# Optimization experiments

Measured on AMD Instinct MI355X. Metric: run time of the kernel, lower is better.

The kernel has to match this reference:

```python
import jax, jax.numpy as jnp
import numpy as np

NH, NB, E, R, K, SU = 64, 384, 1024, 1024, 16, 64  # humans, boxes, enc size, repr size, cardinality, sub-repr
C, P, SPA = 256, 7, 36
NUM_ITER = 2


def _ln(x, g, b):
    m = jnp.mean(x, -1, keepdims=True)
    v = jnp.mean((x - m) ** 2, -1, keepdims=True)
    return (x - m) / jnp.sqrt(v + 1e-5) * g + b


def setup_inputs():
    key = jax.random.key(0)
    it = iter(jax.random.split(key, 48))
    def w(shape, scale=0.02):
        return jax.random.normal(next(it), shape, dtype=jnp.float32) * scale
    z = lambda *s: jnp.zeros(s, jnp.float32)
    return {
        "box_feats": jax.random.normal(next(it), (NB, C, P, P), dtype=jnp.float32),
        "spatial_raw": jax.random.uniform(next(it), (NH * NB, SPA), dtype=jnp.float32),
        "features3": jax.random.normal(next(it), (1, C, P, P), dtype=jnp.float32),
        "Wb1": w((C * P * P, E)), "bb1": z(E), "Wb2": w((E, E)), "bb2": z(E),
        "Ws1": w((SPA, 128)), "bs1": z(128), "Ws2": w((128, 256)), "bs2": z(256),
        "Ws3": w((256, 1024)), "bs3": z(1024),
        "Wadj": w((R, 1)), "badj": z(1),
        "gh": jnp.ones((E,), jnp.float32), "bh": z(E),
        "go": jnp.ones((E,), jnp.float32), "bo": z(E),
        "A1": w((K, 2 * E, SU)), "Ab1": z(K, SU), "A2": w((K, 1024, SU)), "Ab2": z(K, SU),
        "A3": w((K, SU, R)), "Ab3": z(K, R),
        "G1": w((K, 256, SU)), "Gb1": z(K, SU), "G2": w((K, 1024, SU)), "Gb2": z(K, SU),
        "G3": w((K, SU, R)), "Gb3": z(K, R),
        "S1": w((K, E, SU)), "Sb1": z(K, SU), "S2": w((K, 1024, SU)), "Sb2": z(K, SU),
        "S3": w((K, SU, R)), "Sb3": z(K, R),
        "O1": w((K, E, SU)), "Ob1": z(K, SU), "O2": w((K, 1024, SU)), "Ob2": z(K, SU),
        "O3": w((K, SU, R)), "Ob3": z(K, R),
        "n_h": NH,
    }


def _forward(box_feats, spatial_raw, features3, Wb1, bb1, Wb2, bb2, Ws1, bs1, Ws2, bs2, Ws3, bs3,
             Wadj, badj, gh, bh, go, bo, A1, Ab1, A2, Ab2, A3, Ab3, G1, Gb1, G2, Gb2, G3, Gb3,
             S1, Sb1, S2, Sb2, S3, Sb3, O1, Ob1, O2, Ob2, O3, Ob3, n_h):
    n = box_feats.shape[0]
    # box_head: Flatten -> Linear -> ReLU -> Linear -> ReLU
    enc = jax.nn.relu(jax.nn.relu(box_feats.reshape(n, -1) @ Wb1 + bb1) @ Wb2 + bb2)  # [n, E]
    h, o = enc[:n_h], enc
    # spatial_head MLP on flat pairs (pair p = i*n + j, human i, object j)
    sp = spatial_raw
    for W, b in ((Ws1, bs1), (Ws2, bs2), (Ws3, bs3)):
        sp = jax.nn.relu(sp @ W + b)                      # [n_h*n, 1024]
    spr = sp.reshape(n_h, n, -1)
    gfeat = features3.mean((2, 3))                        # AdaptiveAvgPool2d(1) -> [1, 256]

    def mbf(app, W1, b1, W2, b2, W3, b3):
        # MultiBranchFusion over flat pairs, K branches vectorized as batched GEMMs
        a = jnp.einsum('pa,kau->kpu', app, W1) + b1[:, None, :]
        s = jnp.einsum('ps,ksu->kpu', sp, W2) + b2[:, None, :]
        m = jax.nn.relu(a * s)                            # [K, P, sub]
        return jax.nn.relu(jnp.einsum('kpu,kur->pr', m, W3) + b3.sum(0))

    def pair_app(hh, oo):
        return jnp.concatenate([jnp.repeat(hh, n, axis=0), jnp.tile(oo, (n_h, 1))], axis=1)

    adj = jnp.ones((n_h, n), sp.dtype)
    for _ in range(NUM_ITER):
        wts = mbf(pair_app(h, o), A1, Ab1, A2, Ab2, A3, Ab3)      # [P, R]
        adj = (wts @ Wadj + badj).reshape(n_h, n)
        # MessageMBF object->subject (_forward_object_nodes): output [n_h, n, R], no final relu
        ao = jnp.einsum('na,kau->knu', o, O1) + Ob1[:, None, :]
        so = jnp.einsum('hns,ksu->khnu', spr, O2) + Ob2[:, None, None, :]
        m_o2s = jnp.einsum('khnu,kur->hnr', jax.nn.relu(ao[:, None] * so), O3) + Ob3.sum(0)
        h = _ln(h + jax.nn.relu(jnp.sum(jax.nn.softmax(adj, 1)[..., None] * m_o2s, axis=1)), gh, bh)
        # MessageMBF subject->object (_forward_human_nodes): output [n, n_h, R]
        ah = jnp.einsum('ha,kau->khu', h, S1) + Sb1[:, None, :]
        sh = jnp.einsum('hns,ksu->khnu', spr, S2) + Sb2[:, None, None, :]
        m_s2o = jnp.einsum('khnu,kur->nhr', jax.nn.relu(ah[:, :, None, :] * sh), S3) + Sb3.sum(0)
        o = _ln(o + jax.nn.relu(jnp.sum(jax.nn.softmax(adj.T, 1)[..., None] * m_s2o, axis=1)), go, bo)

    attn = mbf(pair_app(h, o), A1, Ab1, A2, Ab2, A3, Ab3)          # [P, R]
    gp = jnp.broadcast_to(gfeat, (sp.shape[0], gfeat.shape[1]))
    attn_g = mbf(gp, G1, Gb1, G2, Gb2, G3, Gb3)                    # [P, R]
    return jnp.concatenate([attn, attn_g], axis=1)                 # [P, 2R]


def reference(box_feats, spatial_raw, features3, Wb1, bb1, Wb2, bb2, Ws1, bs1, Ws2, bs2, Ws3, bs3,
              Wadj, badj, gh, bh, go, bo, A1, Ab1, A2, Ab2, A3, Ab3, G1, Gb1, G2, Gb2, G3, Gb3,
              S1, Sb1, S2, Sb2, S3, Sb3, O1, Ob1, O2, Ob2, O3, Ob3, n_h):
    return _forward(box_feats, spatial_raw, features3, Wb1, bb1, Wb2, bb2, Ws1, bs1, Ws2, bs2, Ws3, bs3,
                    Wadj, badj, gh, bh, go, bo, A1, Ab1, A2, Ab2, A3, Ab3, G1, Gb1, G2, Gb2, G3, Gb3,
                    S1, Sb1, S2, Sb2, S3, Sb3, O1, Ob1, O2, Ob2, O3, Ob3, n_h)
```

## Files before the change

### kernel.cpp

```cpp
#include <hip/hip_runtime.h>
#include <hip/hip_bf16.h>
#include <cstdint>
#include <cstddef>

#define NH    64
#define NB    384
#define EDIM  1024
#define PAIRS (NH*NB)
#define SPA   36

using in_t  = float;
using out_t = float;
using sb_t  = __hip_bfloat16;

typedef short bf16x8 __attribute__((ext_vector_type(8)));
typedef float f32x4  __attribute__((ext_vector_type(4)));

static __device__ __forceinline__ float cvt(float x){ return x; }
static __device__ __forceinline__ float cvt(__hip_bfloat16 x){ return __bfloat162float(x); }
static __device__ __forceinline__ void stv(float* p, float v){ *p = v; }
static __device__ __forceinline__ void stv(__hip_bfloat16* p, float v){ *p = __float2bfloat16(v); }

static __device__ __forceinline__ float b2f(unsigned short u){
  union { unsigned int i; float f; } x; x.i = ((unsigned int)u)<<16; return x.f;
}

typedef const __attribute__((address_space(1))) void* as1_t;
typedef __attribute__((address_space(3))) void* as3_t;
static __device__ __forceinline__ void gl_lds16(const void* g, void* l){
  __builtin_amdgcn_global_load_lds((as1_t)g, (as3_t)l, 16, 0, 0);
}

#define POOL_BB1   0
#define POOL_BB2   1024
#define POOL_BS1   2048
#define POOL_BS2   2176
#define POOL_BS3   2432
#define POOL_AB1   3456
#define POOL_GB1   4480
#define POOL_SB1   5504
#define POOL_OB1   6528
#define POOL_B2ALL 7552
#define POOL_AB3S  11648
#define POOL_GB3S  12672
#define POOL_SB3S  13696
#define POOL_OB3S  14720
#define POOL_GFEAT 15744
#define POOL_TOTAL 16000

template<int EPI, int RELU, typename TC>
__global__ __launch_bounds__(256)
void gemm_mfma(int M, int N, int KS, int lda, int ldb,
               const sb_t* __restrict__ A,
               const sb_t* __restrict__ Bt,
               const float* __restrict__ bias,
               TC* __restrict__ C, int ldc, int coff, long long strideCz,
               const float* __restrict__ Wadj,
               const float* __restrict__ ab3s,
               float* __restrict__ adjOut)
{
  __shared__ alignas(16) short lA[2][128*32];
  __shared__ alignas(16) short lB[2][128*32];
  const int tid = threadIdx.x;
  const int w = tid >> 6, l = tid & 63;
  const int m0 = blockIdx.x * 128, n0 = blockIdx.y * 128;
  const int wr = w >> 1, wc = w & 1;
  const int Koff = blockIdx.z * KS;

  const int srow = w*32 + (l>>2);
  const int scol = (l&3)*8;
  const sb_t* gA = A  + (size_t)(m0 + srow)*(size_t)lda + Koff + scol;
  const sb_t* gB = Bt + (size_t)(n0 + srow)*(size_t)ldb + Koff + scol;
  short* lA0 = &lA[0][(w*32)*32];
  short* lA1 = &lA[1][(w*32)*32];
  short* lB0 = &lB[0][(w*32)*32];
  short* lB1 = &lB[1][(w*32)*32];

  f32x4 acc[4][4];
  const f32x4 zz = {0.f,0.f,0.f,0.f};
  #pragma unroll
  for (int i=0;i<4;++i)
    #pragma unroll
    for (int j=0;j<4;++j) acc[i][j] = zz;

  const int fr  = l & 15;
  const int fko = (l >> 4) * 8;

  for (int k0 = 0; k0 < KS; k0 += 64) {
    gl_lds16(gA + k0,               lA0);
    gl_lds16(gA + k0 + 16*lda,      lA0 + 16*32);
    gl_lds16(gA + k0 + 32,          lA1);
    gl_lds16(gA + k0 + 32 + 16*lda, lA1 + 16*32);
    gl_lds16(gB + k0,               lB0);
    gl_lds16(gB + k0 + 16*ldb,      lB0 + 16*32);
    gl_lds16(gB + k0 + 32,          lB1);
    gl_lds16(gB + k0 + 32 + 16*ldb, lB1 + 16*32);
    __syncthreads();
    #pragma unroll
    for (int kh=0; kh<2; ++kh) {
      bf16x8 af[4], bfv[4];
      #pragma unroll
      for (int i=0;i<4;++i)
        af[i]  = *(const bf16x8*)&lA[kh][(wr*64 + i*16 + fr)*32 + fko];
      #pragma unroll
      for (int j=0;j<4;++j)
        bfv[j] = *(const bf16x8*)&lB[kh][(wc*64 + j*16 + fr)*32 + fko];
      #pragma unroll
      for (int i=0;i<4;++i)
        #pragma unroll
        for (int j=0;j<4;++j)
          acc[i][j] = __builtin_amdgcn_mfma_f32_16x16x32_bf16(af[i], bfv[j], acc[i][j], 0, 0, 0);
    }
    __syncthreads();
  }

  const int cn = l & 15;
  const int cr = (l >> 4) * 4;

  if (EPI == 1) {
    float part[4][4];
    #pragma unroll
    for (int i=0;i<4;++i)
      #pragma unroll
      for (int r=0;r<4;++r) part[i][r] = 0.f;
    #pragma unroll
    for (int j=0;j<4;++j) {
      const int col = n0 + wc*64 + j*16 + cn;
      const float wv = Wadj[col];
      const float bv = ab3s[col];
      #pragma unroll
      for (int i=0;i<4;++i)
        #pragma unroll
        for (int r=0;r<4;++r)
          part[i][r] += fmaxf(acc[i][j][r] + bv, 0.f) * wv;
    }
    #pragma unroll
    for (int m=1;m<16;m<<=1)
      #pragma unroll
      for (int i=0;i<4;++i)
        #pragma unroll
        for (int r=0;r<4;++r)
          part[i][r] += __shfl_xor(part[i][r], m, 64);
    if (cn == 0) {
      #pragma unroll
      for (int i=0;i<4;++i)
        #pragma unroll
        for (int r=0;r<4;++r)
          atomicAdd(&adjOut[m0 + wr*64 + i*16 + cr + r], part[i][r]);
    }
    return;
  }

  #pragma unroll
  for (int j=0;j<4;++j) {
    const int col = n0 + wc*64 + j*16 + cn;
    const float bv = (EPI==0 && bias) ? bias[col] : 0.f;
    #pragma unroll
    for (int i=0;i<4;++i) {
      #pragma unroll
      for (int r=0;r<4;++r) {
        const int row = m0 + wr*64 + i*16 + cr + r;
        float v = acc[i][j][r] + bv;
        if (RELU) v = fmaxf(v, 0.f);
        if (EPI == 2)
          stv(&C[(size_t)blockIdx.z*strideCz + (size_t)row*ldc + col], v);
        else
          stv(&C[(size_t)row*ldc + coff + col], v);
      }
    }
  }
}

template<int EPI, int RELU, typename TC>
__global__ __launch_bounds__(512, 2)
void gemm256(int M, int N, int K, int lda, int ldb,
             const sb_t* __restrict__ A,
             const sb_t* __restrict__ Bt,
             const float* __restrict__ bias,
             TC* __restrict__ C, int ldc, int coff,
             const float* __restrict__ Wadj,
             const float* __restrict__ ab3s,
             float* __restrict__ adjOut)
{
  __shared__ alignas(16) short sh[2][2][256*64];

  const int tid = threadIdx.x;
  const int w = tid >> 6, l = tid & 63;
  const int wr = w >> 2, wc = w & 3;

  const unsigned gx = gridDim.x, gy = gridDim.y;
  const unsigned nwg = gx * gy;
  const unsigned hwid = blockIdx.x + gx * blockIdx.y;
  const unsigned q = nwg >> 3, rr = nwg & 7;
  const unsigned xcd = hwid & 7, jj = hwid >> 3;
  const unsigned wg = (xcd < rr ? xcd*(q+1) : rr*(q+1) + (xcd-rr)*q) + jj;
  const int by = (int)(wg % gy), bx = (int)(wg / gy);
  const int m0 = bx * 256, n0 = by * 256;

  const int NT = K >> 6;

  const int lr = l >> 3;
  const int lch = ((l & 7) ^ lr) * 8;

  auto stage = [&](int p, int s, int t){
    short* lbA = &sh[p][0][0];
    short* lbB = &sh[p][1][0];
    const int k0 = t * 64;
    #pragma unroll
    for (int c=0;c<2;++c){
      const int g = (w<<1) + c;
      int row0; const sb_t* mat; int ld; int rb; short* dst;
      if (s==0){ row0 = g*8;                              mat=Bt; ld=ldb; rb=n0; dst=lbB; }
      else if (s==1){ row0 = 128 + g*8;                   mat=Bt; ld=ldb; rb=n0; dst=lbB; }
      else if (s==2){ row0 = (g<8)? g*8    : 128+(g-8)*8; mat=A;  ld=lda; rb=m0; dst=lbA; }
      else          { row0 = (g<8)? 64+g*8 : 192+(g-8)*8; mat=A;  ld=lda; rb=m0; dst=lbA; }
      gl_lds16(mat + (size_t)(rb + row0 + lr)*(size_t)ld + k0 + lch, dst + row0*64);
    }
  };

  const int fr = l & 15;
  const int fg = l >> 4;
  const int sx = fr & 7;
  const int x0 = ((0 + fg) ^ sx) * 8;
  const int x1 = ((4 + fg) ^ sx) * 8;
  const int oA = (wr*128 + fr) * 64;
  const int oB = (wc*64  + fr) * 64;

  f32x4 acc[8][4];
  const f32x4 zz = {0.f,0.f,0.f,0.f};
  #pragma unroll
  for (int i=0;i<8;++i)
    #pragma unroll
    for (int j=0;j<4;++j) acc[i][j] = zz;

#define G256_BAR()   __builtin_amdgcn_s_barrier()
#define G256_LGKM0() asm volatile("s_waitcnt lgkmcnt(0)" ::: "memory")
#define G256_LGKM8() asm volatile("s_waitcnt lgkmcnt(8)" ::: "memory")
#define G256_VM(n)   asm volatile("s_waitcnt vmcnt(" #n ")" ::: "memory")
#define G256_LOADA(ph)                                                   \
  af[0][0] = *(const bf16x8*)(sa + oA + (2*(ph)+0)*1024 + x0);           \
  af[0][1] = *(const bf16x8*)(sa + oA + (2*(ph)+0)*1024 + x1);           \
  af[1][0] = *(const bf16x8*)(sa + oA + (2*(ph)+1)*1024 + x0);           \
  af[1][1] = *(const bf16x8*)(sa + oA + (2*(ph)+1)*1024 + x1)
#define G256_MFMA(ph)                                                    \
  do { __builtin_amdgcn_s_setprio(1);                                    \
    _Pragma("unroll") for (int kk=0; kk<2; ++kk)                         \
    _Pragma("unroll") for (int ii=0; ii<2; ++ii)                         \
    _Pragma("unroll") for (int j=0; j<4; ++j)                            \
      acc[2*(ph)+ii][j] = __builtin_amdgcn_mfma_f32_16x16x32_bf16(       \
          af[ii][kk], bf[j][kk], acc[2*(ph)+ii][j], 0, 0, 0);            \
    __builtin_amdgcn_s_setprio(0); } while(0)

  stage(0,0,0); stage(0,1,0); stage(0,2,0); stage(0,3,0);
  G256_VM(4);
  if (NT > 1) {
    stage(1,0,1); stage(1,1,1); stage(1,2,1);
    G256_VM(6);
  } else {
    G256_VM(0);
  }
  G256_BAR();

  for (int t=0; t<NT; ++t) {
    const int cur = t & 1, pn = cur ^ 1;
    short* sa  = &sh[cur][0][0];
    short* sb2 = &sh[cur][1][0];
    bf16x8 bf[4][2], af[2][2];

    #pragma unroll
    for (int j=0;j<4;++j){
      bf[j][0] = *(const bf16x8*)(sb2 + oB + j*1024 + x0);
      bf[j][1] = *(const bf16x8*)(sb2 + oB + j*1024 + x1);
    }
    G256_LOADA(0);
    if (t+1 < NT) stage(pn, 3, t+1);
    G256_LGKM8();
    G256_BAR(); G256_LGKM0();
    G256_MFMA(0);
    G256_BAR();

    G256_LOADA(1);
    if (t+2 < NT) stage(cur, 0, t+2);
    G256_BAR(); G256_LGKM0();
    G256_MFMA(1);
    G256_BAR();

    G256_LOADA(2);
    if (t+2 < NT) stage(cur, 1, t+2);
    G256_BAR(); G256_LGKM0();
    G256_MFMA(2);
    G256_BAR();

    G256_LOADA(3);
    if (t+2 < NT) stage(cur, 2, t+2);
    G256_BAR(); G256_LGKM0();
    G256_MFMA(3);
    if (t+1 < NT) {
      if (t+2 < NT) { G256_VM(6); } else { G256_VM(0); }
      G256_BAR();
    }
  }

#undef G256_LOADA
#undef G256_MFMA

  const int cn = l & 15;
  const int cr = (l >> 4) * 4;

  if (EPI == 1) {
    float part[8][4];
    #pragma unroll
    for (int i=0;i<8;++i)
      #pragma unroll
      for (int r=0;r<4;++r) part[i][r] = 0.f;
    #pragma unroll
    for (int j=0;j<4;++j) {
      const int col = n0 + wc*64 + j*16 + cn;
      const float wv = Wadj[col];
      const float bv = ab3s[col];
      #pragma unroll
      for (int i=0;i<8;++i)
        #pragma unroll
        for (int r=0;r<4;++r)
          part[i][r] += fmaxf(acc[i][j][r] + bv, 0.f) * wv;
    }
    #pragma unroll
    for (int m=1;m<16;m<<=1)
      #pragma unroll
      for (int i=0;i<8;++i)
        #pragma unroll
        for (int r=0;r<4;++r)
          part[i][r] += __shfl_xor(part[i][r], m, 64);
    if (cn == 0) {
      #pragma unroll
      for (int i=0;i<8;++i)
        #pragma unroll
        for (int r=0;r<4;++r)
          atomicAdd(&adjOut[m0 + wr*128 + i*16 + cr + r], part[i][r]);
    }
    return;
  }

  if constexpr (sizeof(TC) == 2) {
    sb_t* ebs = (sb_t*)&sh[0][0][0];
    G256_LGKM0();
    G256_BAR();
    #pragma unroll
    for (int i=0;i<8;++i){
      const int lrow = wr*128 + i*16 + cr;
      #pragma unroll
      for (int j=0;j<4;++j){
        const int lcol = wc*64 + j*16 + cn;
        const float bv = bias ? bias[n0 + lcol] : 0.f;
        #pragma unroll
        for (int r=0;r<4;++r){
          float v = acc[i][j][r] + bv;
          if (RELU) v = fmaxf(v, 0.f);
          stv(&ebs[(lrow+r)*256 + lcol], v);
        }
      }
    }
    G256_LGKM0();
    G256_BAR();
    #pragma unroll
    for (int p=0;p<16;++p){
      const int lrow = p*16 + (tid>>5);
      const int sc = (tid&31)*8;
      bf16x8 v = *(const bf16x8*)((const short*)ebs + lrow*256 + sc);
      *(bf16x8*)((short*)C + (size_t)(m0+lrow)*ldc + coff + n0 + sc) = v;
    }
  } else {
    float* ebf = (float*)&sh[0][0][0];
    #pragma unroll
    for (int h=0; h<2; ++h){
      G256_LGKM0();
      G256_BAR();
      if (wr == h){
        #pragma unroll
        for (int i=0;i<8;++i){
          const int lrow = i*16 + cr;
          #pragma unroll
          for (int j=0;j<4;++j){
            const int lcol = wc*64 + j*16 + cn;
            const float bv = bias ? bias[n0 + lcol] : 0.f;
            #pragma unroll
            for (int r=0;r<4;++r){
              float v = acc[i][j][r] + bv;
              if (RELU) v = fmaxf(v, 0.f);
              ebf[(lrow+r)*256 + lcol] = v;
            }
          }
        }
      }
      G256_LGKM0();
      G256_BAR();
      #pragma unroll
      for (int p=0;p<16;++p){
        const int lrow = p*8 + (tid>>6);
        const int sc = (tid&63)*4;
        f32x4 v = *(const f32x4*)&ebf[lrow*256 + sc];
        *(f32x4*)((float*)C + (size_t)(m0 + h*128 + lrow)*ldc + coff + n0 + sc) = v;
      }
    }
  }
#undef G256_BAR
#undef G256_LGKM0
#undef G256_LGKM8
#undef G256_VM
}

template<typename TC>
__global__ __launch_bounds__(256)
void gemm_valu(int M, int N, int K,
               const in_t* __restrict__ S, int ldsS,
               const in_t* __restrict__ B, int ldb, long long strideB,
               const float* __restrict__ bias,
               TC* __restrict__ C, int ldc, int reluOut)
{
  __shared__ float As[16][65];
  __shared__ float Bs[16][68];
  const int z  = blockIdx.z;
  const in_t* Bz = B + (long long)z * strideB;
  const int m0 = blockIdx.x * 64;
  const int n0 = blockIdx.y * 64;
  const int tid = threadIdx.x;
  const int tx = tid & 15;
  const int ty = tid >> 4;

  float acc[4][4];
  #pragma unroll
  for (int i=0;i<4;++i)
    #pragma unroll
    for (int j=0;j<4;++j) acc[i][j]=0.f;

  const int kTiles = (K + 15) >> 4;
  for (int kt=0; kt<kTiles; ++kt) {
    const int k0 = kt << 4;
    #pragma unroll
    for (int q=0;q<4;++q) {
      const int p = m0 + ty + 16*q;
      const int c = k0 + tx;
      As[tx][ty+16*q] = (p < M && c < K) ? S[(size_t)p*ldsS + c] : 0.f;
    }
    {
      const int n = tid & 63;
      #pragma unroll
      for (int q=0;q<4;++q) {
        const int kk = (tid >> 6) + 4*q;
        const int gk = k0 + kk;
        const int gn = n0 + n;
        Bs[kk][n] = (gk < K && gn < N) ? Bz[(size_t)gk*ldb + gn] : 0.f;
      }
    }
    __syncthreads();
    #pragma unroll
    for (int kk=0; kk<16; ++kk) {
      float a[4], b[4];
      #pragma unroll
      for (int i=0;i<4;++i) a[i] = As[kk][ty + 16*i];
      #pragma unroll
      for (int j=0;j<4;++j) b[j] = Bs[kk][tx + 16*j];
      #pragma unroll
      for (int i=0;i<4;++i)
        #pragma unroll
        for (int j=0;j<4;++j) acc[i][j] += a[i]*b[j];
    }
    __syncthreads();
  }
  #pragma unroll
  for (int i=0;i<4;++i) {
    const int r = m0 + ty + 16*i;
    if (r >= M) continue;
    #pragma unroll
    for (int j=0;j<4;++j) {
      const int nn = n0 + tx + 16*j;
      if (nn >= N) continue;
      const int ccol = z*N + nn;
      float v = acc[i][j];
      if (bias) v += bias[ccol];
      if (reluOut) v = fmaxf(v, 0.f);
      stv(&C[(size_t)r*ldc + ccol], v);
    }
  }
}

struct Prep17 { const in_t* p[17]; };

__global__ __launch_bounds__(256)
void prep_kernel(Prep17 a, float* __restrict__ pool)
{
  const int len[17] = {1024,1024,128,256,1024,1024,1024,1024,1024,1024,1024,1024,1024,
                       1024,1024,1024,1024};
  const int off[17] = {POOL_BB1,POOL_BB2,POOL_BS1,POOL_BS2,POOL_BS3,POOL_AB1,
                       POOL_B2ALL+0,
                       POOL_GB1,
                       POOL_B2ALL+3072,
                       POOL_SB1,
                       POOL_B2ALL+2048,
                       POOL_OB1,
                       POOL_B2ALL+1024,
                       POOL_AB3S,POOL_GB3S,POOL_SB3S,POOL_OB3S};
  const int j = blockIdx.x;
  const in_t* src = a.p[j];
  const int L = len[j], o = off[j];
  for (int i = threadIdx.x; i < L; i += blockDim.x) {
    if (j < 13) {
      pool[o+i] = src[i];
    } else {
      float s = 0.f;
      for (int k=0;k<16;++k) s += src[k*1024 + i];
      pool[o+i] = s;
    }
  }
}

__global__ __launch_bounds__(64)
void gfeat_kernel(const in_t* __restrict__ f3, float* __restrict__ g)
{
  const int c = blockIdx.x;
  const int t = threadIdx.x;
  float s = (t < 49) ? f3[c*49 + t] : 0.f;
  #pragma unroll
  for (int o=32;o>0;o>>=1) s += __shfl_down(s, o, 64);
  if (t == 0) g[c] = s * (1.0f/49.0f);
}

__global__ __launch_bounds__(256)
void tcvt_kernel(const float* __restrict__ in, sb_t* __restrict__ outT, int R, int C)
{
  __shared__ float t[64][65];
  const int r0 = blockIdx.x*64, c0 = blockIdx.y*64;
  const int x = threadIdx.x & 63, y = threadIdx.x >> 6;
  #pragma unroll 4
  for (int q=0;q<16;++q){ const int rl = q*4 + y; t[rl][x] = in[(size_t)(r0+rl)*C + c0 + x]; }
  __syncthreads();
  #pragma unroll 4
  for (int q=0;q<16;++q){ const int cl = q*4 + y; stv(&outT[(size_t)(c0+cl)*R + r0 + x], t[x][cl]); }
}

__global__ __launch_bounds__(256)
void pack_kt_kernel(const float* __restrict__ W, sb_t* __restrict__ PT, int Cdim)
{
  __shared__ float t[64][65];
  const int c0 = blockIdx.x*64; const int k = blockIdx.y;
  const int x = threadIdx.x & 63, y = threadIdx.x >> 6;
  #pragma unroll 4
  for (int q=0;q<16;++q){ const int cl = q*4 + y; t[cl][x] = W[((size_t)k*Cdim + c0 + cl)*64 + x]; }
  __syncthreads();
  #pragma unroll 4
  for (int q=0;q<16;++q){ const int u = q*4 + y; stv(&PT[((size_t)k*64 + u)*Cdim + c0 + x], t[x][u]); }
}

__global__ void cvt_kernel(const float* __restrict__ in, sb_t* __restrict__ o, int n){
  const int i = blockIdx.x*256 + threadIdx.x;
  if (i < n) stv(&o[i], in[i]);
}

__global__ __launch_bounds__(256)
void combine4_kernel(const float* __restrict__ part, const float* __restrict__ bias,
                     sb_t* __restrict__ o)
{
  const int i = blockIdx.x*256 + threadIdx.x;
  const int c = i & 1023;
  float v = part[i] + part[i+393216] + part[i+2*393216] + part[i+3*393216] + bias[c];
  stv(&o[i], fmaxf(v, 0.f));
}

__global__ __launch_bounds__(256)
void combineN_kernel(const float* __restrict__ part, long long stride, int nz,
                     const float* __restrict__ bias, int N, int relu,
                     float* __restrict__ out)
{
  const int i = blockIdx.x*256 + threadIdx.x;
  float v = bias ? bias[i & (N-1)] : 0.f;
  for (int z=0; z<nz; ++z) v += part[(long long)z*stride + i];
  if (relu) v = fmaxf(v, 0.f);
  out[i] = v;
}

__global__ __launch_bounds__(256)
void encpost_kernel(const float* __restrict__ oB, sb_t* __restrict__ oBb,
                    float* __restrict__ hB, sb_t* __restrict__ hBb)
{
  const int p = blockIdx.x; const int c = blockIdx.y*256 + threadIdx.x;
  const float v = oB[(size_t)p*1024 + c];
  stv(&oBb[(size_t)p*1024+c], v);
  if (p < NH){ hB[(size_t)p*1024+c] = v; stv(&hBb[(size_t)p*1024+c], v); }
}

__global__ __launch_bounds__(256)
void mmake_kernel(const float* __restrict__ U, int hasU, int ldu,
                  const float* __restrict__ V, int hasV,
                  const sb_t* __restrict__ S, int ldS, int colOff,
                  sb_t* __restrict__ Mo)
{
  const int p = blockIdx.x;
  const int c = threadIdx.x * 4;
  const ushort4 sv = *(const ushort4*)((const unsigned short*)S + (size_t)p*ldS + colOff + c);
  float a0=0.f,a1=0.f,a2=0.f,a3=0.f;
  if (hasU){ const float* Up = U + (size_t)(p/NB)*ldu + c; a0=Up[0];a1=Up[1];a2=Up[2];a3=Up[3]; }
  if (hasV){ const float* Vp = V + (size_t)(p%NB)*1024 + c; a0+=Vp[0];a1+=Vp[1];a2+=Vp[2];a3+=Vp[3]; }
  __hip_bfloat16* mo = (__hip_bfloat16*)Mo + (size_t)p*1024 + c;
  mo[0] = __float2bfloat16(fmaxf(a0*b2f(sv.x),0.f));
  mo[1] = __float2bfloat16(fmaxf(a1*b2f(sv.y),0.f));
  mo[2] = __float2bfloat16(fmaxf(a2*b2f(sv.z),0.f));
  mo[3] = __float2bfloat16(fmaxf(a3*b2f(sv.w),0.f));
}

__global__ __launch_bounds__(512)
void smax_h_kernel(const float* __restrict__ adj, float* __restrict__ wh)
{
  __shared__ float red[512];
  const int hh = blockIdx.x, t = threadIdx.x;
  float av = (t < NB) ? adj[hh*NB + t] : -1e30f;
  red[t]=av; __syncthreads();
  for (int s=256;s>0;s>>=1){ if(t<s) red[t]=fmaxf(red[t],red[t+s]); __syncthreads(); }
  float mx = red[0]; __syncthreads();
  float e = (t < NB) ? __expf(av - mx) : 0.f;
  red[t]=e; __syncthreads();
  for (int s=256;s>0;s>>=1){ if(t<s) red[t]+=red[t+s]; __syncthreads(); }
  if (t < NB) wh[hh*NB + t] = e / red[0];
}

__global__ __launch_bounds__(64)
void smax_o_kernel(const float* __restrict__ adj, float* __restrict__ wo)
{
  const int n = blockIdx.x, t = threadIdx.x;
  float av = adj[t*NB + n];
  float mx = av;
  #pragma unroll
  for (int o=32;o>0;o>>=1) mx = fmaxf(mx, __shfl_xor(mx, o, 64));
  float e = __expf(av - mx);
  float s = e;
  #pragma unroll
  for (int o=32;o>0;o>>=1) s += __shfl_xor(s, o, 64);
  wo[n*64 + t] = e / s;
}

__global__ __launch_bounds__(128)
void wredH_kernel(const float* __restrict__ wh, const float* __restrict__ ao,
                  const sb_t* __restrict__ s4, int colOff, sb_t* __restrict__ mw)
{
  const int hh = blockIdx.x;
  const int c = blockIdx.y*128 + threadIdx.x;
  const unsigned short* sp = (const unsigned short*)s4 + (size_t)hh*NB*4096 + colOff + c;
  const float* whp = wh + hh*NB;
  float acc = 0.f;
  for (int n=0; n<NB; ++n)
    acc += whp[n] * fmaxf(ao[(size_t)n*1024 + c] * b2f(sp[(size_t)n*4096]), 0.f);
  stv(&mw[(size_t)hh*1024 + c], acc);
}

__global__ __launch_bounds__(128)
void wredO_kernel(const float* __restrict__ wo, const float* __restrict__ ah,
                  const sb_t* __restrict__ s4, int colOff, sb_t* __restrict__ mw)
{
  const int n = blockIdx.x;
  const int c = blockIdx.y*128 + threadIdx.x;
  const unsigned short* sp = (const unsigned short*)s4 + (size_t)n*4096 + colOff + c;
  const float* wop = wo + n*64;
  float acc = 0.f;
  for (int h=0; h<NH; ++h)
    acc += wop[h] * fmaxf(ah[(size_t)h*1024 + c] * b2f(sp[(size_t)h*NB*4096]), 0.f);
  stv(&mw[(size_t)n*1024 + c], acc);
}

static __device__ __forceinline__ float bsum(float v, float* red){
  const int t = threadIdx.x;
  red[t]=v; __syncthreads();
  for (int s=512;s>0;s>>=1){ if(t<s) red[t]+=red[t+s]; __syncthreads(); }
  float r = red[0]; __syncthreads();
  return r;
}

__global__ __launch_bounds__(1024)
void ln_update_kernel(const float* __restrict__ msg, const float* __restrict__ b3s,
                      const in_t* __restrict__ g, const in_t* __restrict__ b,
                      float* __restrict__ x, sb_t* __restrict__ xb)
{
  __shared__ float red[1024];
  const int row = blockIdx.x, t = threadIdx.x;
  float val = x[(size_t)row*1024 + t] + fmaxf(msg[(size_t)row*1024 + t] + b3s[t], 0.f);
  float mean = bsum(val, red) * (1.0f/1024.0f);
  float d = val - mean;
  float var = bsum(d*d, red) * (1.0f/1024.0f);
  float y = d * rsqrtf(var + 1e-5f) * g[t] + b[t];
  x[(size_t)row*1024 + t] = y;
  stv(&xb[(size_t)row*1024 + t], y);
}

template<int EPI, int RELU, typename TC>
static inline void launch_mfma(hipStream_t st, int M, int N, int KS, int lda, int ldb, int nz,
    const sb_t* A, const sb_t* Bt, const float* bias, TC* C, int ldc, int coff,
    long long strideCz, const float* Wadj, const float* ab3s, float* adjOut)
{
  dim3 g((unsigned)(M/128), (unsigned)(N/128), (unsigned)nz);
  hipLaunchKernelGGL((gemm_mfma<EPI,RELU,TC>), g, dim3(256), 0, st,
                     M,N,KS,lda,ldb,A,Bt,bias,C,ldc,coff,strideCz,Wadj,ab3s,adjOut);
}

template<int EPI, int RELU, typename TC>
static inline void launch_mfma256(hipStream_t st, int M, int N, int K, int lda, int ldb,
    const sb_t* A, const sb_t* Bt, const float* bias, TC* C, int ldc, int coff,
    const float* Wadj, const float* ab3s, float* adjOut)
{
  dim3 g((unsigned)(M/256), (unsigned)(N/256), 1);
  hipLaunchKernelGGL((gemm256<EPI,RELU,TC>), g, dim3(512), 0, st,
                     M,N,K,lda,ldb,A,Bt,bias,C,ldc,coff,Wadj,ab3s,adjOut);
}

static inline void launch_skinny(hipStream_t st, int M, int N, int K, int lda, int ldb, int nz,
    const sb_t* A, const sb_t* Bt, const float* bias, float* outp, int relu, float* scratch)
{
  launch_mfma<2,0,float>(st, M, N, K/nz, lda, ldb, nz, A, Bt, nullptr, scratch, N, 0,
                         (long long)M*N, nullptr, nullptr, nullptr);
  hipLaunchKernelGGL(combineN_kernel, dim3((unsigned)((M*N)/256)), dim3(256), 0, st,
                     scratch, (long long)M*N, nz, bias, N, relu, outp);
}

extern "C" void kernel_launch(void* const* d_in, const int* in_sizes, int n_in,
                              void* d_out, int out_size, void* d_ws, size_t ws_size,
                              hipStream_t stream)
{
  (void)in_sizes; (void)n_in; (void)out_size; (void)ws_size;

  const in_t* box  = (const in_t*)d_in[0];
  const in_t* spat = (const in_t*)d_in[1];
  const in_t* f3   = (const in_t*)d_in[2];
  const in_t* Wb1  = (const in_t*)d_in[3];
  const in_t* Wb2  = (const in_t*)d_in[5];
  const in_t* Ws1  = (const in_t*)d_in[7];
  const in_t* Ws2  = (const in_t*)d_in[9];
  const in_t* Ws3  = (const in_t*)d_in[11];
  const in_t* Wadj = (const in_t*)d_in[13];
  const in_t* gh   = (const in_t*)d_in[15];
  const in_t* bh   = (const in_t*)d_in[16];
  const in_t* go   = (const in_t*)d_in[17];
  const in_t* bo   = (const in_t*)d_in[18];
  const in_t* A1   = (const in_t*)d_in[19];
  const in_t* A2   = (const in_t*)d_in[21];
  const in_t* A3   = (const in_t*)d_in[23];
  const in_t* G1   = (const in_t*)d_in[25];
  const in_t* G2   = (const in_t*)d_in[27];
  const in_t* G3   = (const in_t*)d_in[29];
  const in_t* S1   = (const in_t*)d_in[31];
  const in_t* S2   = (const in_t*)d_in[33];
  const in_t* S3   = (const in_t*)d_in[35];
  const in_t* O1   = (const in_t*)d_in[37];
  const in_t* O2   = (const in_t*)d_in[39];
  const in_t* O3   = (const in_t*)d_in[41];
  out_t* out = (out_t*)d_out;

  char* wsb = (char*)d_ws;
  size_t off = 0;
  auto alloc = [&](size_t bytes)->void* {
    void* p = wsb + off; off += (bytes + 255) & ~(size_t)255; return p;
  };
  float* pool   = (float*)alloc((size_t)POOL_TOTAL*4);
  sb_t* Wb1T    = (sb_t*)alloc((size_t)1024*12544*2);
  sb_t* Wb2T    = (sb_t*)alloc((size_t)1024*1024*2);
  sb_t* Ws2T    = (sb_t*)alloc((size_t)256*128*2);
  sb_t* Ws3T    = (sb_t*)alloc((size_t)1024*256*2);
  sb_t* A3T     = (sb_t*)alloc((size_t)1024*1024*2);
  sb_t* O3T     = (sb_t*)alloc((size_t)1024*1024*2);
  sb_t* S3T     = (sb_t*)alloc((size_t)1024*1024*2);
  sb_t* G3T     = (sb_t*)alloc((size_t)1024*1024*2);
  sb_t* s2Tall  = (sb_t*)alloc((size_t)4096*1024*2);
  sb_t* O1T     = (sb_t*)alloc((size_t)1024*1024*2);
  sb_t* S1T     = (sb_t*)alloc((size_t)1024*1024*2);
  sb_t* A1T     = (sb_t*)alloc((size_t)1024*2048*2);
  sb_t* boxb    = (sb_t*)alloc((size_t)NB*12544*2);
  float* encP   = (float*)alloc((size_t)4*NB*EDIM*4);
  sb_t* encMidb = (sb_t*)alloc((size_t)NB*EDIM*2);
  float* oB     = (float*)alloc((size_t)NB*EDIM*4);
  sb_t* oBb     = (sb_t*)alloc((size_t)NB*EDIM*2);
  float* hB     = (float*)alloc((size_t)NH*EDIM*4);
  sb_t* hBb     = (sb_t*)alloc((size_t)128*EDIM*2);
  sb_t* sp1b    = (sb_t*)alloc((size_t)PAIRS*128*2);
  sb_t* sp2b    = (sb_t*)alloc((size_t)PAIRS*256*2);
  sb_t* spFb    = (sb_t*)alloc((size_t)PAIRS*EDIM*2);
  sb_t* mbuf    = spFb;
  sb_t* s4      = (sb_t*)alloc((size_t)PAIRS*4096*2);
  float* ahA    = (float*)alloc((size_t)128*EDIM*4);
  float* aoA    = (float*)alloc((size_t)NB*EDIM*4);
  float* aoO    = (float*)alloc((size_t)NB*EDIM*4);
  float* ahS    = (float*)alloc((size_t)128*EDIM*4);
  float* aGv    = (float*)alloc((size_t)EDIM*4);
  float* adj    = (float*)alloc((size_t)PAIRS*4);
  float* wh     = (float*)alloc((size_t)PAIRS*4);
  float* wo     = (float*)alloc((size_t)PAIRS*4);
  sb_t* mwH     = (sb_t*)alloc((size_t)128*EDIM*2);
  sb_t* mwO     = (sb_t*)alloc((size_t)NB*EDIM*2);
  float* hmsg   = (float*)alloc((size_t)128*EDIM*4);
  float* omsg   = (float*)alloc((size_t)NB*EDIM*4);

  Prep17 pp;
  const int prepIdx[17] = {4,6,8,10,12,20,22,26,28,32,34,38,40,24,30,36,42};
  for (int i=0;i<17;++i) pp.p[i] = (const in_t*)d_in[prepIdx[i]];
  hipLaunchKernelGGL(prep_kernel, dim3(17), dim3(256), 0, stream, pp, pool);
  hipLaunchKernelGGL(gfeat_kernel, dim3(256), dim3(64), 0, stream, f3, pool + POOL_GFEAT);

  hipLaunchKernelGGL(tcvt_kernel, dim3(196,16), dim3(256), 0, stream, Wb1, Wb1T, 12544, 1024);
  hipLaunchKernelGGL(tcvt_kernel, dim3(16,16),  dim3(256), 0, stream, Wb2, Wb2T, 1024, 1024);
  hipLaunchKernelGGL(tcvt_kernel, dim3(2,4),    dim3(256), 0, stream, Ws2, Ws2T, 128, 256);
  hipLaunchKernelGGL(tcvt_kernel, dim3(4,16),   dim3(256), 0, stream, Ws3, Ws3T, 256, 1024);
  hipLaunchKernelGGL(tcvt_kernel, dim3(16,16),  dim3(256), 0, stream, A3, A3T, 1024, 1024);
  hipLaunchKernelGGL(tcvt_kernel, dim3(16,16),  dim3(256), 0, stream, O3, O3T, 1024, 1024);
  hipLaunchKernelGGL(tcvt_kernel, dim3(16,16),  dim3(256), 0, stream, S3, S3T, 1024, 1024);
  hipLaunchKernelGGL(tcvt_kernel, dim3(16,16),  dim3(256), 0, stream, G3, G3T, 1024, 1024);

  hipLaunchKernelGGL(pack_kt_kernel, dim3(16,16), dim3(256), 0, stream, A2, s2Tall,            1024);
  hipLaunchKernelGGL(pack_kt_kernel, dim3(16,16), dim3(256), 0, stream, O2, s2Tall+1024*1024,  1024);
  hipLaunchKernelGGL(pack_kt_kernel, dim3(16,16), dim3(256), 0, stream, S2, s2Tall+2048*1024,  1024);
  hipLaunchKernelGGL(pack_kt_kernel, dim3(16,16), dim3(256), 0, stream, G2, s2Tall+3072*1024,  1024);
  hipLaunchKernelGGL(pack_kt_kernel, dim3(16,16), dim3(256), 0, stream, O1, O1T, 1024);
  hipLaunchKernelGGL(pack_kt_kernel, dim3(16,16), dim3(256), 0, stream, S1, S1T, 1024);
  hipLaunchKernelGGL(pack_kt_kernel, dim3(32,16), dim3(256), 0, stream, A1, A1T, 2048);

  hipLaunchKernelGGL(cvt_kernel, dim3((NB*12544)/256), dim3(256), 0, stream, box, boxb, NB*12544);

  launch_mfma<2,0,float>(stream, NB, EDIM, 3136, 12544, 12544, 4,
      boxb, Wb1T, nullptr, encP, EDIM, 0, (long long)NB*EDIM, nullptr, nullptr, nullptr);
  hipLaunchKernelGGL(combine4_kernel, dim3(NB*EDIM/256), dim3(256), 0, stream,
                     encP, pool+POOL_BB1, encMidb);
  launch_skinny(stream, NB, EDIM, EDIM, EDIM, EDIM, 4,
      encMidb, Wb2T, pool+POOL_BB2, oB, 1, encP);
  hipLaunchKernelGGL(encpost_kernel, dim3(NB,4), dim3(256), 0, stream, oB, oBb, hB, hBb);

  {
    dim3 g((PAIRS+63)/64, 2, 1);
    hipLaunchKernelGGL((gemm_valu<sb_t>), g, dim3(256), 0, stream,
        PAIRS, 128, SPA, spat, SPA, Ws1, 128, 0, pool+POOL_BS1, sp1b, 128, 1);
  }
  launch_mfma<0,1,sb_t>(stream, PAIRS, 256, 128, 128, 128, 1,
      sp1b, Ws2T, pool+POOL_BS2, sp2b, 256, 0, 0, nullptr, nullptr, nullptr);
  launch_mfma256<0,1,sb_t>(stream, PAIRS, EDIM, 256, 256, 256,
      sp2b, Ws3T, pool+POOL_BS3, spFb, EDIM, 0, nullptr, nullptr, nullptr);

  launch_mfma256<0,0,sb_t>(stream, PAIRS, 4096, EDIM, EDIM, EDIM,
      spFb, s2Tall, pool+POOL_B2ALL, s4, 4096, 0, nullptr, nullptr, nullptr);

  {
    dim3 g(1, 1, 16);
    hipLaunchKernelGGL((gemm_valu<float>), g, dim3(256), 0, stream,
        1, 64, 256, pool+POOL_GFEAT, 256, G1, 64, 16384, pool+POOL_GB1, aGv, EDIM, 0);
  }

  for (int it=0; it<2; ++it) {
    launch_skinny(stream, 128, EDIM, EDIM, EDIM, 2048, 8,
        hBb, A1T, pool+POOL_AB1, ahA, 0, encP);
    launch_skinny(stream, NB, EDIM, EDIM, EDIM, 2048, 4,
        oBb, A1T+1024, nullptr, aoA, 0, encP);
    hipLaunchKernelGGL(mmake_kernel, dim3(PAIRS), dim3(256), 0, stream,
                       ahA, 1, 1024, aoA, 1, s4, 4096, 0, mbuf);
    (void)hipMemsetAsync(adj, 0, (size_t)PAIRS*4, stream);
    launch_mfma256<1,0,float>(stream, PAIRS, EDIM, EDIM, EDIM, EDIM,
        mbuf, A3T, nullptr, (float*)nullptr, 0, 0, Wadj, pool+POOL_AB3S, adj);
    hipLaunchKernelGGL(smax_h_kernel, dim3(NH), dim3(512), 0, stream, adj, wh);
    hipLaunchKernelGGL(smax_o_kernel, dim3(NB), dim3(64), 0, stream, adj, wo);

    launch_skinny(stream, NB, EDIM, EDIM, EDIM, 1024, 4,
        oBb, O1T, pool+POOL_OB1, aoO, 0, encP);
    hipLaunchKernelGGL(wredH_kernel, dim3(NH,8), dim3(128), 0, stream,
                       wh, aoO, s4, 1024, mwH);
    launch_skinny(stream, 128, EDIM, EDIM, EDIM, 1024, 8,
        mwH, O3T, nullptr, hmsg, 0, encP);
    hipLaunchKernelGGL(ln_update_kernel, dim3(NH), dim3(1024), 0, stream,
                       hmsg, pool+POOL_OB3S, gh, bh, hB, hBb);

    launch_skinny(stream, 128, EDIM, EDIM, EDIM, 1024, 8,
        hBb, S1T, pool+POOL_SB1, ahS, 0, encP);
    hipLaunchKernelGGL(wredO_kernel, dim3(NB,8), dim3(128), 0, stream,
                       wo, ahS, s4, 2048, mwO);
    launch_skinny(stream, NB, EDIM, EDIM, EDIM, 1024, 4,
        mwO, S3T, nullptr, omsg, 0, encP);
    hipLaunchKernelGGL(ln_update_kernel, dim3(NB), dim3(1024), 0, stream,
                       omsg, pool+POOL_SB3S, go, bo, oB, oBb);
  }

  launch_skinny(stream, 128, EDIM, EDIM, EDIM, 2048, 8,
      hBb, A1T, pool+POOL_AB1, ahA, 0, encP);
  launch_skinny(stream, NB, EDIM, EDIM, EDIM, 2048, 4,
      oBb, A1T+1024, nullptr, aoA, 0, encP);
  hipLaunchKernelGGL(mmake_kernel, dim3(PAIRS), dim3(256), 0, stream,
                     ahA, 1, 1024, aoA, 1, s4, 4096, 0, mbuf);
  launch_mfma256<0,1,out_t>(stream, PAIRS, EDIM, EDIM, EDIM, EDIM,
      mbuf, A3T, pool+POOL_AB3S, out, 2048, 0, nullptr, nullptr, nullptr);

  hipLaunchKernelGGL(mmake_kernel, dim3(PAIRS), dim3(256), 0, stream,
                     aGv, 1, 0, nullptr, 0, s4, 4096, 3072, mbuf);
  launch_mfma256<0,1,out_t>(stream, PAIRS, EDIM, EDIM, EDIM, EDIM,
      mbuf, G3T, pool+POOL_GB3S, out, 2048, 1024, nullptr, nullptr, nullptr);
}
```

Baseline: 1.481 ms.

## Switch 256-tile GEMM to 32x32x16 MFMA, swizzle epilogue LDS, split-K 7

The 256x256 GEMM kernel now uses 32x32x16 bf16 MFMA instructions with 16-float accumulators instead of 16x16x32. It reorganizes the fragment loads, the adjacency epilogue reduction, and the output staging to match the new accumulator layout. Epilogue LDS writes and reads are XOR-swizzled to reduce bank conflicts. Separately, the box-head first GEMM is split seven ways instead of four, and a generic combine kernel replaces the specialized one. This trades more partial-sum traffic for more parallelism.

```diff
diff --git a/kernel.cpp b/kernel.cpp
--- a/kernel.cpp
+++ b/kernel.cpp
@@ -15,6 +15,7 @@
 
 typedef short bf16x8 __attribute__((ext_vector_type(8)));
 typedef float f32x4  __attribute__((ext_vector_type(4)));
+typedef float f32x16 __attribute__((ext_vector_type(16)));
 
 static __device__ __forceinline__ float cvt(float x){ return x; }
 static __device__ __forceinline__ float cvt(__hip_bfloat16 x){ return __bfloat162float(x); }
@@ -218,37 +219,35 @@
     }
   };
 
-  const int fr = l & 15;
-  const int fg = l >> 4;
+  const int fr = l & 31;
+  const int fg = l >> 5;
   const int sx = fr & 7;
-  const int x0 = ((0 + fg) ^ sx) * 8;
-  const int x1 = ((4 + fg) ^ sx) * 8;
+  const int kx[4] = { (((0)+fg) ^ sx) * 8, (((2)+fg) ^ sx) * 8,
+                      (((4)+fg) ^ sx) * 8, (((6)+fg) ^ sx) * 8 };
   const int oA = (wr*128 + fr) * 64;
   const int oB = (wc*64  + fr) * 64;
 
-  f32x4 acc[8][4];
-  const f32x4 zz = {0.f,0.f,0.f,0.f};
+  f32x16 acc[4][2];
   #pragma unroll
-  for (int i=0;i<8;++i)
-    #pragma unroll
-    for (int j=0;j<4;++j) acc[i][j] = zz;
+  for (int i=0;i<4;++i)
+    #pragma unroll
+    for (int j=0;j<2;++j)
+      #pragma unroll
+      for (int r=0;r<16;++r) acc[i][j][r] = 0.f;
 
 #define G256_BAR()   __builtin_amdgcn_s_barrier()
 #define G256_LGKM0() asm volatile("s_waitcnt lgkmcnt(0)" ::: "memory")
 #define G256_LGKM8() asm volatile("s_waitcnt lgkmcnt(8)" ::: "memory")
 #define G256_VM(n)   asm volatile("s_waitcnt vmcnt(" #n ")" ::: "memory")
 #define G256_LOADA(ph)                                                   \
-  af[0][0] = *(const bf16x8*)(sa + oA + (2*(ph)+0)*1024 + x0);           \
-  af[0][1] = *(const bf16x8*)(sa + oA + (2*(ph)+0)*1024 + x1);           \
-  af[1][0] = *(const bf16x8*)(sa + oA + (2*(ph)+1)*1024 + x0);           \
-  af[1][1] = *(const bf16x8*)(sa + oA + (2*(ph)+1)*1024 + x1)
+  _Pragma("unroll") for (int kk=0; kk<4; ++kk)                           \
+    af[kk] = *(const bf16x8*)(sa + oA + (ph)*2048 + kx[kk]);
 #define G256_MFMA(ph)                                                    \
   do { __builtin_amdgcn_s_setprio(1);                                    \
-    _Pragma("unroll") for (int kk=0; kk<2; ++kk)                         \
-    _Pragma("unroll") for (int ii=0; ii<2; ++ii)                         \
-    _Pragma("unroll") for (int j=0; j<4; ++j)                            \
-      acc[2*(ph)+ii][j] = __builtin_amdgcn_mfma_f32_16x16x32_bf16(       \
-          af[ii][kk], bf[j][kk], acc[2*(ph)+ii][j], 0, 0, 0);            \
+    _Pragma("unroll") for (int kk=0; kk<4; ++kk)                         \
+    _Pragma("unroll") for (int ni=0; ni<2; ++ni)                         \
+      acc[(ph)][ni] = __builtin_amdgcn_mfma_f32_32x32x16_bf16(           \
+          af[kk], bf[ni][kk], acc[(ph)][ni], 0, 0, 0);                   \
     __builtin_amdgcn_s_setprio(0); } while(0)
 
   stage(0,0,0); stage(0,1,0); stage(0,2,0); stage(0,3,0);
@@ -265,13 +264,13 @@
     const int cur = t & 1, pn = cur ^ 1;
     short* sa  = &sh[cur][0][0];
     short* sb2 = &sh[cur][1][0];
-    bf16x8 bf[4][2], af[2][2];
-
-    #pragma unroll
-    for (int j=0;j<4;++j){
-      bf[j][0] = *(const bf16x8*)(sb2 + oB + j*1024 + x0);
-      bf[j][1] = *(const bf16x8*)(sb2 + oB + j*1024 + x1);
-    }
+    bf16x8 bf[2][4], af[4];
+
+    #pragma unroll
+    for (int ni=0;ni<2;++ni)
+      #pragma unroll
+      for (int kk=0;kk<4;++kk)
+        bf[ni][kk] = *(const bf16x8*)(sb2 + oB + ni*2048 + kx[kk]);
     G256_LOADA(0);
     if (t+1 < NT) stage(pn, 3, t+1);
     G256_LGKM8();
@@ -304,39 +303,37 @@
 #undef G256_LOADA
 #undef G256_MFMA
 
-  const int cn = l & 15;
-  const int cr = (l >> 4) * 4;
-
   if (EPI == 1) {
-    float part[8][4];
-    #pragma unroll
-    for (int i=0;i<8;++i)
-      #pragma unroll
-      for (int r=0;r<4;++r) part[i][r] = 0.f;
-    #pragma unroll
-    for (int j=0;j<4;++j) {
-      const int col = n0 + wc*64 + j*16 + cn;
+    float part[4][16];
+    #pragma unroll
+    for (int i=0;i<4;++i)
+      #pragma unroll
+      for (int r=0;r<16;++r) part[i][r] = 0.f;
+    #pragma unroll
+    for (int ni=0;ni<2;++ni) {
+      const int col = n0 + wc*64 + ni*32 + fr;
       const float wv = Wadj[col];
       const float bv = ab3s[col];
       #pragma unroll
-      for (int i=0;i<8;++i)
-        #pragma unroll
-        for (int r=0;r<4;++r)
-          part[i][r] += fmaxf(acc[i][j][r] + bv, 0.f) * wv;
-    }
-    #pragma unroll
-    for (int m=1;m<16;m<<=1)
-      #pragma unroll
-      for (int i=0;i<8;++i)
-        #pragma unroll
-        for (int r=0;r<4;++r)
+      for (int i=0;i<4;++i)
+        #pragma unroll
+        for (int r=0;r<16;++r)
+          part[i][r] += fmaxf(acc[i][ni][r] + bv, 0.f) * wv;
+    }
+    #pragma unroll
+    for (int m=1;m<32;m<<=1)
+      #pragma unroll
+      for (int i=0;i<4;++i)
+        #pragma unroll
+        for (int r=0;r<16;++r)
           part[i][r] += __shfl_xor(part[i][r], m, 64);
-    if (cn == 0) {
-      #pragma unroll
-      for (int i=0;i<8;++i)
-        #pragma unroll
-        for (int r=0;r<4;++r)
-          atomicAdd(&adjOut[m0 + wr*128 + i*16 + cr + r], part[i][r]);
+    if (fr == 0) {
+      #pragma unroll
+      for (int i=0;i<4;++i)
+        #pragma unroll
+        for (int r=0;r<16;++r)
+          atomicAdd(&adjOut[m0 + wr*128 + i*32 + (r&3) + 8*(r>>2) + 4*fg],
+                    part[i][r]);
     }
     return;
   }
@@ -346,17 +343,18 @@
     G256_LGKM0();
     G256_BAR();
     #pragma unroll
-    for (int i=0;i<8;++i){
-      const int lrow = wr*128 + i*16 + cr;
-      #pragma unroll
-      for (int j=0;j<4;++j){
-        const int lcol = wc*64 + j*16 + cn;
+    for (int i=0;i<4;++i){
+      #pragma unroll
+      for (int ni=0;ni<2;++ni){
+        const int lcol = wc*64 + ni*32 + fr;
         const float bv = bias ? bias[n0 + lcol] : 0.f;
-        #pragma unroll
-        for (int r=0;r<4;++r){
-          float v = acc[i][j][r] + bv;
+        const int cb = lcol >> 3, ce = lcol & 7;
+        #pragma unroll
+        for (int r=0;r<16;++r){
+          const int lrow = wr*128 + i*32 + (r&3) + 8*(r>>2) + 4*fg;
+          float v = acc[i][ni][r] + bv;
           if (RELU) v = fmaxf(v, 0.f);
-          stv(&ebs[(lrow+r)*256 + lcol], v);
+          stv(&ebs[lrow*256 + ((cb ^ (lrow & 7)) << 3) + ce], v);
         }
       }
     }
@@ -364,10 +362,10 @@
     G256_BAR();
     #pragma unroll
     for (int p=0;p<16;++p){
-      const int lrow = p*16 + (tid>>5);
-      const int sc = (tid&31)*8;
-      bf16x8 v = *(const bf16x8*)((const short*)ebs + lrow*256 + sc);
-      *(bf16x8*)((short*)C + (size_t)(m0+lrow)*ldc + coff + n0 + sc) = v;
+      const int R = p*16 + (tid>>5);
+      const int c = tid & 31;
+      bf16x8 v = *(const bf16x8*)((const short*)ebs + R*256 + ((c ^ (R & 7)) << 3));
+      *(bf16x8*)((short*)C + (size_t)(m0+R)*ldc + coff + n0 + c*8) = v;
     }
   } else {
     float* ebf = (float*)&sh[0][0][0];
@@ -377,17 +375,18 @@
       G256_BAR();
       if (wr == h){
         #pragma unroll
-        for (int i=0;i<8;++i){
-          const int lrow = i*16 + cr;
+        for (int i=0;i<4;++i){
           #pragma unroll
-          for (int j=0;j<4;++j){
-            const int lcol = wc*64 + j*16 + cn;
+          for (int ni=0;ni<2;++ni){
+            const int lcol = wc*64 + ni*32 + fr;
             const float bv = bias ? bias[n0 + lcol] : 0.f;
+            const int cb = lcol >> 2, ce = lcol & 3;
             #pragma unroll
-            for (int r=0;r<4;++r){
-              float v = acc[i][j][r] + bv;
+            for (int r=0;r<16;++r){
+              const int lrow = i*32 + (r&3) + 8*(r>>2) + 4*fg;
+              float v = acc[i][ni][r] + bv;
               if (RELU) v = fmaxf(v, 0.f);
-              ebf[(lrow+r)*256 + lcol] = v;
+              ebf[lrow*256 + ((cb ^ (lrow & 7)) << 2) + ce] = v;
             }
           }
         }
@@ -396,10 +395,10 @@
       G256_BAR();
       #pragma unroll
       for (int p=0;p<16;++p){
-        const int lrow = p*8 + (tid>>6);
-        const int sc = (tid&63)*4;
-        f32x4 v = *(const f32x4*)&ebf[lrow*256 + sc];
-        *(f32x4*)((float*)C + (size_t)(m0 + h*128 + lrow)*ldc + coff + n0 + sc) = v;
+        const int R = p*8 + (tid>>6);
+        const int c = tid & 63;
+        f32x4 v = *(const f32x4*)&ebf[R*256 + ((c ^ (R & 7)) << 2)];
+        *(f32x4*)((float*)C + (size_t)(m0 + h*128 + R)*ldc + coff + n0 + c*4) = v;
       }
     }
   }
@@ -556,26 +555,17 @@
   if (i < n) stv(&o[i], in[i]);
 }
 
-__global__ __launch_bounds__(256)
-void combine4_kernel(const float* __restrict__ part, const float* __restrict__ bias,
-                     sb_t* __restrict__ o)
-{
-  const int i = blockIdx.x*256 + threadIdx.x;
-  const int c = i & 1023;
-  float v = part[i] + part[i+393216] + part[i+2*393216] + part[i+3*393216] + bias[c];
-  stv(&o[i], fmaxf(v, 0.f));
-}
-
+template<typename TO>
 __global__ __launch_bounds__(256)
 void combineN_kernel(const float* __restrict__ part, long long stride, int nz,
                      const float* __restrict__ bias, int N, int relu,
-                     float* __restrict__ out)
+                     TO* __restrict__ out)
 {
   const int i = blockIdx.x*256 + threadIdx.x;
   float v = bias ? bias[i & (N-1)] : 0.f;
   for (int z=0; z<nz; ++z) v += part[(long long)z*stride + i];
   if (relu) v = fmaxf(v, 0.f);
-  out[i] = v;
+  stv(&out[i], v);
 }
 
 __global__ __launch_bounds__(256)
@@ -714,7 +704,7 @@
 {
   launch_mfma<2,0,float>(st, M, N, K/nz, lda, ldb, nz, A, Bt, nullptr, scratch, N, 0,
                          (long long)M*N, nullptr, nullptr, nullptr);
-  hipLaunchKernelGGL(combineN_kernel, dim3((unsigned)((M*N)/256)), dim3(256), 0, st,
+  hipLaunchKernelGGL((combineN_kernel<float>), dim3((unsigned)((M*N)/256)), dim3(256), 0, st,
                      scratch, (long long)M*N, nz, bias, N, relu, outp);
 }
 
@@ -770,7 +760,7 @@
   sb_t* S1T     = (sb_t*)alloc((size_t)1024*1024*2);
   sb_t* A1T     = (sb_t*)alloc((size_t)1024*2048*2);
   sb_t* boxb    = (sb_t*)alloc((size_t)NB*12544*2);
-  float* encP   = (float*)alloc((size_t)4*NB*EDIM*4);
+  float* encP   = (float*)alloc((size_t)7*NB*EDIM*4);
   sb_t* encMidb = (sb_t*)alloc((size_t)NB*EDIM*2);
   float* oB     = (float*)alloc((size_t)NB*EDIM*4);
   sb_t* oBb     = (sb_t*)alloc((size_t)NB*EDIM*2);
@@ -819,10 +809,10 @@
 
   hipLaunchKernelGGL(cvt_kernel, dim3((NB*12544)/256), dim3(256), 0, stream, box, boxb, NB*12544);
 
-  launch_mfma<2,0,float>(stream, NB, EDIM, 3136, 12544, 12544, 4,
+  launch_mfma<2,0,float>(stream, NB, EDIM, 1792, 12544, 12544, 7,
       boxb, Wb1T, nullptr, encP, EDIM, 0, (long long)NB*EDIM, nullptr, nullptr, nullptr);
-  hipLaunchKernelGGL(combine4_kernel, dim3(NB*EDIM/256), dim3(256), 0, stream,
-                     encP, pool+POOL_BB1, encMidb);
+  hipLaunchKernelGGL((combineN_kernel<sb_t>), dim3(NB*EDIM/256), dim3(256), 0, stream,
+                     encP, (long long)NB*EDIM, 7, pool+POOL_BB1, EDIM, 1, encMidb);
   launch_skinny(stream, NB, EDIM, EDIM, EDIM, EDIM, 4,
       encMidb, Wb2T, pool+POOL_BB2, oB, 1, encP);
   hipLaunchKernelGGL(encpost_kernel, dim3(NB,4), dim3(256), 0, stream, oB, oBb, hB, hBb);
```

Measured after the change: 1.551 ms. +4.7%, slower.

## Swizzle gemm256 epilogue LDS staging and raise box-head split-K to 7

Applied to the files above, without the earlier changes.

The gemm256 epilogue now writes its staging tile to LDS with an XOR swizzle on 8-element (bf16) or 4-element (fp32) column blocks keyed by row, and reads it back with the matching swizzle. This is meant to reduce LDS bank conflicts when scattering MFMA accumulators into shared memory. Separately, the first box-head GEMM now splits K into 7 slices instead of 4, which gives more workgroups for the small-M problem. The fixed-4 combine kernel is replaced by a templated combineN that reduces 7 partials, at the cost of more scratch memory and partial-sum traffic.

```diff
diff --git a/kernel.cpp b/kernel.cpp
--- a/kernel.cpp
+++ b/kernel.cpp
@@ -347,16 +347,17 @@
     G256_BAR();
     #pragma unroll
     for (int i=0;i<8;++i){
-      const int lrow = wr*128 + i*16 + cr;
       #pragma unroll
       for (int j=0;j<4;++j){
         const int lcol = wc*64 + j*16 + cn;
         const float bv = bias ? bias[n0 + lcol] : 0.f;
+        const int cb = lcol >> 3, ce = lcol & 7;
         #pragma unroll
         for (int r=0;r<4;++r){
+          const int lrow = wr*128 + i*16 + cr + r;
           float v = acc[i][j][r] + bv;
           if (RELU) v = fmaxf(v, 0.f);
-          stv(&ebs[(lrow+r)*256 + lcol], v);
+          stv(&ebs[lrow*256 + ((cb ^ (lrow & 7)) << 3) + ce], v);
         }
       }
     }
@@ -364,10 +365,10 @@
     G256_BAR();
     #pragma unroll
     for (int p=0;p<16;++p){
-      const int lrow = p*16 + (tid>>5);
-      const int sc = (tid&31)*8;
-      bf16x8 v = *(const bf16x8*)((const short*)ebs + lrow*256 + sc);
-      *(bf16x8*)((short*)C + (size_t)(m0+lrow)*ldc + coff + n0 + sc) = v;
+      const int R = p*16 + (tid>>5);
+      const int c = tid & 31;
+      bf16x8 v = *(const bf16x8*)((const short*)ebs + R*256 + ((c ^ (R & 7)) << 3));
+      *(bf16x8*)((short*)C + (size_t)(m0+R)*ldc + coff + n0 + c*8) = v;
     }
   } else {
     float* ebf = (float*)&sh[0][0][0];
@@ -378,16 +379,17 @@
       if (wr == h){
         #pragma unroll
         for (int i=0;i<8;++i){
-          const int lrow = i*16 + cr;
           #pragma unroll
           for (int j=0;j<4;++j){
             const int lcol = wc*64 + j*16 + cn;
             const float bv = bias ? bias[n0 + lcol] : 0.f;
+            const int cb = lcol >> 2, ce = lcol & 3;
             #pragma unroll
             for (int r=0;r<4;++r){
+              const int lrow = i*16 + cr + r;
               float v = acc[i][j][r] + bv;
               if (RELU) v = fmaxf(v, 0.f);
-              ebf[(lrow+r)*256 + lcol] = v;
+              ebf[lrow*256 + ((cb ^ (lrow & 7)) << 2) + ce] = v;
             }
           }
         }
@@ -396,10 +398,10 @@
       G256_BAR();
       #pragma unroll
       for (int p=0;p<16;++p){
-        const int lrow = p*8 + (tid>>6);
-        const int sc = (tid&63)*4;
-        f32x4 v = *(const f32x4*)&ebf[lrow*256 + sc];
-        *(f32x4*)((float*)C + (size_t)(m0 + h*128 + lrow)*ldc + coff + n0 + sc) = v;
+        const int R = p*8 + (tid>>6);
+        const int c = tid & 63;
+        f32x4 v = *(const f32x4*)&ebf[R*256 + ((c ^ (R & 7)) << 2)];
+        *(f32x4*)((float*)C + (size_t)(m0 + h*128 + R)*ldc + coff + n0 + c*4) = v;
       }
     }
   }
@@ -556,26 +558,17 @@
   if (i < n) stv(&o[i], in[i]);
 }
 
-__global__ __launch_bounds__(256)
-void combine4_kernel(const float* __restrict__ part, const float* __restrict__ bias,
-                     sb_t* __restrict__ o)
-{
-  const int i = blockIdx.x*256 + threadIdx.x;
-  const int c = i & 1023;
-  float v = part[i] + part[i+393216] + part[i+2*393216] + part[i+3*393216] + bias[c];
-  stv(&o[i], fmaxf(v, 0.f));
-}
-
+template<typename TO>
 __global__ __launch_bounds__(256)
 void combineN_kernel(const float* __restrict__ part, long long stride, int nz,
                      const float* __restrict__ bias, int N, int relu,
-                     float* __restrict__ out)
+                     TO* __restrict__ out)
 {
   const int i = blockIdx.x*256 + threadIdx.x;
   float v = bias ? bias[i & (N-1)] : 0.f;
   for (int z=0; z<nz; ++z) v += part[(long long)z*stride + i];
   if (relu) v = fmaxf(v, 0.f);
-  out[i] = v;
+  stv(&out[i], v);
 }
 
 __global__ __launch_bounds__(256)
@@ -714,7 +707,7 @@
 {
   launch_mfma<2,0,float>(st, M, N, K/nz, lda, ldb, nz, A, Bt, nullptr, scratch, N, 0,
                          (long long)M*N, nullptr, nullptr, nullptr);
-  hipLaunchKernelGGL(combineN_kernel, dim3((unsigned)((M*N)/256)), dim3(256), 0, st,
+  hipLaunchKernelGGL((combineN_kernel<float>), dim3((unsigned)((M*N)/256)), dim3(256), 0, st,
                      scratch, (long long)M*N, nz, bias, N, relu, outp);
 }
 
@@ -770,7 +763,7 @@
   sb_t* S1T     = (sb_t*)alloc((size_t)1024*1024*2);
   sb_t* A1T     = (sb_t*)alloc((size_t)1024*2048*2);
   sb_t* boxb    = (sb_t*)alloc((size_t)NB*12544*2);
-  float* encP   = (float*)alloc((size_t)4*NB*EDIM*4);
+  float* encP   = (float*)alloc((size_t)7*NB*EDIM*4);
   sb_t* encMidb = (sb_t*)alloc((size_t)NB*EDIM*2);
   float* oB     = (float*)alloc((size_t)NB*EDIM*4);
   sb_t* oBb     = (sb_t*)alloc((size_t)NB*EDIM*2);
@@ -819,10 +812,10 @@
 
   hipLaunchKernelGGL(cvt_kernel, dim3((NB*12544)/256), dim3(256), 0, stream, box, boxb, NB*12544);
 
-  launch_mfma<2,0,float>(stream, NB, EDIM, 3136, 12544, 12544, 4,
+  launch_mfma<2,0,float>(stream, NB, EDIM, 1792, 12544, 12544, 7,
       boxb, Wb1T, nullptr, encP, EDIM, 0, (long long)NB*EDIM, nullptr, nullptr, nullptr);
-  hipLaunchKernelGGL(combine4_kernel, dim3(NB*EDIM/256), dim3(256), 0, stream,
-                     encP, pool+POOL_BB1, encMidb);
+  hipLaunchKernelGGL((combineN_kernel<sb_t>), dim3(NB*EDIM/256), dim3(256), 0, stream,
+                     encP, (long long)NB*EDIM, 7, pool+POOL_BB1, EDIM, 1, encMidb);
   launch_skinny(stream, NB, EDIM, EDIM, EDIM, EDIM, 4,
       encMidb, Wb2T, pool+POOL_BB2, oB, 1, encP);
   hipLaunchKernelGGL(encpost_kernel, dim3(NB,4), dim3(256), 0, stream, oB, oBb, hB, hBb);
```

Result: no change. 1.482 ms (+0.1%).
